# Optimization experiments

Measured on AMD Instinct MI355X. Metric: run time of the kernel, lower is better.

Reference implementation:

```python
import jax, jax.numpy as jnp
import numpy as np

N = 100000   # graph nodes
E = 600000   # edges
D = 128      # feature_dim
K = 3        # candidate ops per MixedOp
EPS = 1e-5   # BatchNorm eps


def _param_stack(key, n_ops):
    kW, kb = jax.random.split(key)
    W = jax.random.normal(kW, (n_ops, K, D, D), jnp.float32) * (1.0 / np.sqrt(D))
    b = jax.random.normal(kb, (n_ops, K, D), jnp.float32) * 0.01
    g = jnp.ones((n_ops, K, D), jnp.float32)
    be = jnp.zeros((n_ops, K, D), jnp.float32)
    return W, b, g, be


def setup_inputs() -> dict:
    key = jax.random.key(0)
    ks = jax.random.split(key, 16)
    inp = {
        'src_emb': jax.random.normal(ks[0], (N, D), jnp.float32),
        'hr': jax.random.normal(ks[1], (N, D), jnp.float32),
        'edge_src': jax.random.randint(ks[2], (E,), 0, N),
        'edge_dst': jax.random.randint(ks[3], (E,), 0, N),
        'weights_zero': jax.random.uniform(ks[4], (1, K), jnp.float32),
        'weights_first': jax.random.uniform(ks[5], (3, K), jnp.float32),
        'weights_middle': jax.random.uniform(ks[6], (2, K), jnp.float32),
        'weights_last': jax.random.uniform(ks[7], (2, K), jnp.float32),
    }
    for name, k, n_ops in [('zero', ks[8], 1), ('first', ks[9], 3), ('mid', ks[10], 2), ('last', ks[11], 2)]:
        W, b, g, be = _param_stack(k, n_ops)
        inp[f'W_{name}'] = W; inp[f'b_{name}'] = b
        inp[f'g_{name}'] = g; inp[f'be_{name}'] = be
    inp['W_cat'] = jax.random.normal(ks[12], (3 * D, D), jnp.float32) * (1.0 / np.sqrt(3 * D))
    inp['b_cat'] = jax.random.normal(ks[13], (D,), jnp.float32) * 0.01
    inp['g_cat'] = jnp.ones((D,), jnp.float32)
    inp['be_cat'] = jnp.zeros((D,), jnp.float32)
    return inp


def _mean_agg(h, src, dst):
    s = jax.ops.segment_sum(h[src], dst, num_segments=N)            # [N,D]
    deg = jax.ops.segment_sum(jnp.ones((src.shape[0],), h.dtype), dst, num_segments=N)
    return s / jnp.maximum(deg, 1.0)[:, None]


def _max_agg(h, src, dst):
    m = jax.ops.segment_max(h[src], dst, num_segments=N)            # -inf for empty segs
    return jnp.where(jnp.isfinite(m), m, 0.0)


def _mixed(cands, w, W, b, g, be):
    # cands: list of K [N,D]; w:[K]; W:[K,D,D]; b/g/be:[K,D]
    x = jnp.stack(cands)                                            # [K,N,D]
    y = jnp.einsum('knd,kdf->knf', x, W) + b[:, None, :]            # Linear per candidate
    mu = jnp.mean(y, axis=1, keepdims=True)                         # BatchNorm1d (batch stats)
    var = jnp.var(y, axis=1, keepdims=True)
    y = (y - mu) * jax.lax.rsqrt(var + EPS) * g[:, None, :] + be[:, None, :]
    y = jax.nn.relu(y)
    return jnp.einsum('k,knd->nd', w, y)                            # alpha-weighted sum


def _graph_cands(h, src, dst):
    return [h, _mean_agg(h, src, dst), _max_agg(h, src, dst)]


def _cell_forward(src_emb, hr, edge_src, edge_dst,
                  weights_zero, weights_first, weights_middle, weights_last,
                  W_zero, b_zero, g_zero, be_zero,
                  W_first, b_first, g_first, be_first,
                  W_mid, b_mid, g_mid, be_mid,
                  W_last, b_last, g_last, be_last,
                  W_cat, b_cat, g_cat, be_cat):
    src, dst = edge_src, edge_dst
    # Cell_Zero: relation-composition candidates on (src_emb, hr)
    pre = [src_emb, src_emb - hr, src_emb * hr]
    h_in = _mixed(pre, weights_zero[0], W_zero[0], b_zero[0], g_zero[0], be_zero[0])
    # Cell_First (nodes=2): ops layout [(i=0,j=0),(i=1,j=0),(i=1,j=1)]
    states = [h_in]
    s0 = _mixed(_graph_cands(states[0], src, dst), weights_first[0], W_first[0], b_first[0], g_first[0], be_first[0])
    states.append(s0)
    s1 = (_mixed(_graph_cands(states[0], src, dst), weights_first[1], W_first[1], b_first[1], g_first[1], be_first[1])
          + _mixed(_graph_cands(states[1], src, dst), weights_first[2], W_first[2], b_first[2], g_first[2], be_first[2]))
    states.append(s1)
    states = states[1:]                                             # drop h_in -> len 2
    # Cell_Middle (nodes=2): one MixedOp per state
    states = [_mixed(_graph_cands(states[i], src, dst), weights_middle[i], W_mid[i], b_mid[i], g_mid[i], be_mid[i])
              for i in range(2)]
    # Cell_Last (in_nodes=2, nodes=1): one new state from both inputs; returns all 3
    s_last = (_mixed(_graph_cands(states[0], src, dst), weights_last[0], W_last[0], b_last[0], g_last[0], be_last[0])
              + _mixed(_graph_cands(states[1], src, dst), weights_last[1], W_last[1], b_last[1], g_last[1], be_last[1]))
    states = states + [s_last]                                      # len 3
    # concat -> Linear -> BN -> ReLU (dropout p=0)
    h = jnp.concatenate(states, axis=1) @ W_cat + b_cat             # [N,D]
    mu = jnp.mean(h, axis=0, keepdims=True)
    var = jnp.var(h, axis=0, keepdims=True)
    h = (h - mu) * jax.lax.rsqrt(var + EPS) * g_cat + be_cat
    return jax.nn.relu(h)


def reference(src_emb, hr, edge_src, edge_dst,
              weights_zero, weights_first, weights_middle, weights_last,
              W_zero, b_zero, g_zero, be_zero,
              W_first, b_first, g_first, be_first,
              W_mid, b_mid, g_mid, be_mid,
              W_last, b_last, g_last, be_last,
              W_cat, b_cat, g_cat, be_cat):
    return _cell_forward(src_emb, hr, edge_src, edge_dst,
                         weights_zero, weights_first, weights_middle, weights_last,
                         W_zero, b_zero, g_zero, be_zero,
                         W_first, b_first, g_first, be_first,
                         W_mid, b_mid, g_mid, be_mid,
                         W_last, b_last, g_last, be_last,
                         W_cat, b_cat, g_cat, be_cat)
```

## Files before the change

### kernel.cpp

```cpp
#include <hip/hip_runtime.h>

#define N_NODES 100000
#define N_EDGES 600000
#define NPAD    100096
#define NTILES  782
#define SCAN_B  98
#define EPS_F   1e-5f
#define GRIDG   256

typedef __bf16 bf16_t;
typedef __bf16 bf16x8 __attribute__((ext_vector_type(8)));
typedef __bf16 bf16x4 __attribute__((ext_vector_type(4)));
typedef float  f32x4  __attribute__((ext_vector_type(4)));

__global__ __launch_bounds__(256)
void init_zero_kernel(int* __restrict__ deg, int* __restrict__ cnt)
{
    int i = blockIdx.x * 256 + threadIdx.x;
    if (i < N_NODES) deg[i] = 0;
    if (i < 32) cnt[i] = 0;
}

__global__ __launch_bounds__(256)
void transpose_w_kernel(const float* __restrict__ Wz, const float* __restrict__ Wf,
                        const float* __restrict__ Wm, const float* __restrict__ Wl,
                        const float* __restrict__ Wc, bf16_t* __restrict__ wt)
{
    int idx = blockIdx.x * 256 + threadIdx.x;
    int mat = idx >> 14;
    int off = idx & 16383;
    int n = off >> 7, kk = off & 127;
    const float* src;
    if      (mat < 3)  src = Wz + mat * 16384;
    else if (mat < 12) src = Wf + (mat - 3) * 16384;
    else if (mat < 18) src = Wm + (mat - 12) * 16384;
    else if (mat < 24) src = Wl + (mat - 18) * 16384;
    else               src = Wc + (mat - 24) * 16384;
    wt[idx] = (bf16_t)src[kk * 128 + n];
}

__global__ __launch_bounds__(256)
void pre_kernel(const float* __restrict__ se, const float* __restrict__ hr,
                bf16_t* __restrict__ p0, bf16_t* __restrict__ p1, bf16_t* __restrict__ p2)
{
    long i = ((long)blockIdx.x * 256 + threadIdx.x) * 8;
    float4 a0 = *(const float4*)&se[i], a1 = *(const float4*)&se[i + 4];
    float4 b0 = *(const float4*)&hr[i], b1 = *(const float4*)&hr[i + 4];
    float av[8] = {a0.x, a0.y, a0.z, a0.w, a1.x, a1.y, a1.z, a1.w};
    float bv[8] = {b0.x, b0.y, b0.z, b0.w, b1.x, b1.y, b1.z, b1.w};
    bf16x8 o0, o1, o2;
#pragma unroll
    for (int j = 0; j < 8; ++j) {
        o0[j] = (bf16_t)av[j];
        o1[j] = (bf16_t)(av[j] - bv[j]);
        o2[j] = (bf16_t)(av[j] * bv[j]);
    }
    *(bf16x8*)&p0[i] = o0;
    *(bf16x8*)&p1[i] = o1;
    *(bf16x8*)&p2[i] = o2;
}

__global__ __launch_bounds__(256)
void deg_count_kernel(const int* __restrict__ dst, int* __restrict__ deg)
{
    int i = blockIdx.x * 256 + threadIdx.x;
    if (i < N_EDGES) atomicAdd(&deg[dst[i]], 1);
}

__global__ __launch_bounds__(256)
void scan_a_kernel(const int* __restrict__ deg, int* __restrict__ partials)
{
    __shared__ int ls[256];
    int b = blockIdx.x, t = threadIdx.x;
    int s = 0;
    for (int j = 0; j < 4; ++j) {
        int i = b * 1024 + t * 4 + j;
        if (i < N_NODES) s += deg[i];
    }
    ls[t] = s; __syncthreads();
    for (int o = 128; o > 0; o >>= 1) {
        if (t < o) ls[t] += ls[t + o];
        __syncthreads();
    }
    if (t == 0) partials[b] = ls[0];
}

__global__ void scan_b_kernel(const int* __restrict__ partials, int* __restrict__ pofs)
{
    if (threadIdx.x == 0) {
        int a = 0;
        for (int i = 0; i < SCAN_B; ++i) { pofs[i] = a; a += partials[i]; }
    }
}

__global__ __launch_bounds__(256)
void scan_c_kernel(const int* __restrict__ deg, const int* __restrict__ pofs,
                   int* __restrict__ row_ptr, int* __restrict__ cursor)
{
    __shared__ int ls[256];
    int b = blockIdx.x, t = threadIdx.x;
    int v[4], s = 0;
    for (int j = 0; j < 4; ++j) {
        int i = b * 1024 + t * 4 + j;
        v[j] = (i < N_NODES) ? deg[i] : 0;
        s += v[j];
    }
    ls[t] = s; __syncthreads();
    for (int o = 1; o < 256; o <<= 1) {
        int tv = (t >= o) ? ls[t - o] : 0;
        __syncthreads();
        ls[t] += tv;
        __syncthreads();
    }
    int excl = ls[t] - s + pofs[b];
    for (int j = 0; j < 4; ++j) {
        int i = b * 1024 + t * 4 + j;
        if (i < N_NODES) { row_ptr[i] = excl; cursor[i] = excl; excl += v[j]; }
    }
    if (b == 0 && t == 0) row_ptr[N_NODES] = N_EDGES;
}

__global__ __launch_bounds__(256)
void scatter_kernel(const int* __restrict__ src, const int* __restrict__ dst,
                    int* __restrict__ cursor, int* __restrict__ csr_src)
{
    int i = blockIdx.x * 256 + threadIdx.x;
    if (i < N_EDGES) {
        int p = atomicAdd(&cursor[dst[i]], 1);
        csr_src[p] = src[i];
    }
}

__global__ __launch_bounds__(256)
void agg_kernel(const bf16_t* __restrict__ h, const int* __restrict__ row_ptr,
                const int* __restrict__ csr_src,
                bf16_t* __restrict__ mean_o, bf16_t* __restrict__ max_o)
{
    int node = blockIdx.x * 16 + (threadIdx.x >> 4);
    int dd = (threadIdx.x & 15) * 8;
    int e0 = row_ptr[node], e1 = row_ptr[node + 1];
    float s[8], mx[8];
#pragma unroll
    for (int j = 0; j < 8; ++j) { s[j] = 0.f; mx[j] = 0.f; }
    for (int e = e0; e < e1; ++e) {
        int sc = csr_src[e];
        bf16x8 v = *(const bf16x8*)&h[(long)sc * 128 + dd];
#pragma unroll
        for (int j = 0; j < 8; ++j) {
            float f = (float)v[j];
            s[j] += f;
            mx[j] = fmaxf(mx[j], f);
        }
    }
    float inv = 1.f / fmaxf((float)(e1 - e0), 1.f);
    bf16x8 om, ox;
#pragma unroll
    for (int j = 0; j < 8; ++j) { om[j] = (bf16_t)(s[j] * inv); ox[j] = (bf16_t)mx[j]; }
    *(bf16x8*)&mean_o[(long)node * 128 + dd] = om;
    *(bf16x8*)&max_o [(long)node * 128 + dd] = ox;
}

__device__ __forceinline__ void gload_lds16(const bf16_t* g, bf16_t* l)
{
    __builtin_amdgcn_global_load_lds(
        (const __attribute__((address_space(1))) void*)g,
        (__attribute__((address_space(3))) void*)l, 16, 0, 0);
}

__device__ __forceinline__ void barrier_lgkm()
{
    asm volatile("s_waitcnt lgkmcnt(0)" ::: "memory");
    __builtin_amdgcn_s_barrier();
    asm volatile("" ::: "memory");
}

__device__ __forceinline__ void grid_bar(int* c, int do_rel, int do_acq)
{
    __syncthreads();
    if (threadIdx.x == 0) {
        if (do_rel) __builtin_amdgcn_fence(__ATOMIC_RELEASE, "agent");
        __hip_atomic_fetch_add(c, 1, __ATOMIC_RELAXED, __HIP_MEMORY_SCOPE_AGENT);
        while (__hip_atomic_load(c, __ATOMIC_RELAXED, __HIP_MEMORY_SCOPE_AGENT) < GRIDG)
            __builtin_amdgcn_s_sleep(16);
        if (do_acq) __builtin_amdgcn_fence(__ATOMIC_ACQUIRE, "agent");
    }
    __syncthreads();
}

__global__ __launch_bounds__(512, 1)
void mixed_kernel(const bf16_t* __restrict__ x0, const bf16_t* __restrict__ x1,
                  const bf16_t* __restrict__ x2, const bf16_t* __restrict__ wt,
                  const float* __restrict__ bias, const float* __restrict__ gg,
                  const float* __restrict__ be, const float* __restrict__ wmix,
                  bf16_t* __restrict__ outb, float* __restrict__ outf,
                  float* __restrict__ partial, float* __restrict__ tmp,
                  int* __restrict__ cnt, int mode, int accflag)
{
    __shared__ __align__(16) bf16_t lds_x[4][16384];
    __shared__ float lsc[768];

    const int tid  = threadIdx.x;
    const int lane = tid & 63;
    const int w8   = tid >> 6;
    const int quad = lane >> 4;
    const int t16  = lane & 15;
    const int wr = w8 >> 2, wc = w8 & 3;
    const int bid = blockIdx.x;
    const float invN = 1.0f / (float)N_NODES;

    int srcoff[4], dsto[4];
#pragma unroll
    for (int i = 0; i < 4; ++i) {
        int ci = i * 512 + tid;
        int row = ci >> 4, c = ci & 15;
        srcoff[i] = row * 128 + ((c ^ (row & 15)) * 8);
        dsto[i]   = ci * 8;
    }
    auto stage = [&](const bf16_t* src, int slot) {
#pragma unroll
        for (int i = 0; i < 4; ++i)
            gload_lds16(src + srcoff[i], &lds_x[slot][dsto[i]]);
    };
    auto xp = [&](int c) { return (c == 0) ? x0 : (c == 1) ? x1 : x2; };

    bf16x8 wreg[3][2][4];
#pragma unroll
    for (int c = 0; c < 3; ++c)
#pragma unroll
        for (int ns = 0; ns < 2; ++ns)
#pragma unroll
            for (int ks = 0; ks < 4; ++ks)
                wreg[c][ns][ks] = *(const bf16x8*)
                    &wt[(long)c * 16384 + (wc * 32 + ns * 16 + t16) * 128
                        + ks * 32 + quad * 8];

    const int ts = (int)(((long)bid * NTILES) / GRIDG);
    const int te = (int)(((long)(bid + 1) * NTILES) / GRIDG);
    const int nk = (mode == 0) ? 3 : 1;

    f32x4 acc[2][4];
    float ssA[3][8], sqA[3][8];
#pragma unroll
    for (int k = 0; k < 3; ++k)
#pragma unroll
        for (int i = 0; i < 8; ++i) { ssA[k][i] = 0.f; sqA[k][i] = 0.f; }

#define ZACC() do { \
    _Pragma("unroll") for (int a_ = 0; a_ < 2; ++a_) \
    _Pragma("unroll") for (int b_ = 0; b_ < 4; ++b_) \
        acc[a_][b_] = (f32x4){0.f, 0.f, 0.f, 0.f}; } while (0)

#define MMAC(C) do { \
    _Pragma("unroll") for (int ks = 0; ks < 4; ++ks) { \
        bf16x8 xf[4]; \
        _Pragma("unroll") for (int ms = 0; ms < 4; ++ms) { \
            int row_ = wr * 64 + ms * 16 + t16; \
            int sw_ = (ks * 4 + quad) ^ t16; \
            xf[ms] = *(const bf16x8*)&lds_x[slot][row_ * 128 + sw_ * 8]; \
        } \
        _Pragma("unroll") for (int ns = 0; ns < 2; ++ns) \
        _Pragma("unroll") for (int ms = 0; ms < 4; ++ms) \
            acc[ns][ms] = __builtin_amdgcn_mfma_f32_16x16x32_bf16( \
                wreg[C][ns][ks], xf[ms], acc[ns][ms], 0, 0, 0); \
    } } while (0)

#define ACCST(K) do { \
    _Pragma("unroll") for (int ms = 0; ms < 4; ++ms) { \
        long m_ = (long)tile * 128 + wr * 64 + ms * 16 + t16; \
        if (m_ < N_NODES) { \
            _Pragma("unroll") for (int ns = 0; ns < 2; ++ns) \
            _Pragma("unroll") for (int j_ = 0; j_ < 4; ++j_) { \
                float v_ = acc[ns][ms][j_]; \
                ssA[K][ns * 4 + j_] += v_; \
                sqA[K][ns * 4 + j_] += v_ * v_; \
            } \
        } \
    } } while (0)

#define RINGWAIT(w_, e_) do { \
    int ah_ = (e_) - 1 - (w_); \
    if (ah_ >= 2)      asm volatile("s_waitcnt vmcnt(8)" ::: "memory"); \
    else if (ah_ == 1) asm volatile("s_waitcnt vmcnt(4)" ::: "memory"); \
    else               asm volatile("s_waitcnt vmcnt(0)" ::: "memory"); \
    __builtin_amdgcn_sched_barrier(0); \
    __builtin_amdgcn_s_barrier(); \
    __builtin_amdgcn_sched_barrier(0); } while (0)

    {
        int sA, eA;
        if (mode == 0) {
            sA = (int)(((long)bid * (NTILES * 3)) / GRIDG);
            eA = (int)(((long)(bid + 1) * (NTILES * 3)) / GRIDG);
        } else {
            sA = ts * 3; eA = te * 3;
        }
#pragma unroll 1
        for (int i = 0; i < 3; ++i)
            if (sA + i < eA) stage(xp((sA + i) % 3) + (long)((sA + i) / 3) * 16384,
                                   (sA + i) & 3);
#pragma unroll 1
        for (int w = sA; w < eA; ++w) {
            const int c = w % 3, tile = w / 3, slot = w & 3;
            RINGWAIT(w, eA);
            if (w + 3 < eA)
                stage(xp((w + 3) % 3) + (long)((w + 3) / 3) * 16384, (w + 3) & 3);
            if (mode == 0 || c == 0) ZACC();
            if (c == 0) MMAC(0); else if (c == 1) MMAC(1); else MMAC(2);
            if (mode == 0) {
                if (c == 0) ACCST(0); else if (c == 1) ACCST(1); else ACCST(2);
            } else if (c == 2) ACCST(0);
        }
    }

#pragma unroll
    for (int o = 1; o < 16; o <<= 1)
#pragma unroll
        for (int k = 0; k < 3; ++k)
#pragma unroll
            for (int i = 0; i < 8; ++i) {
                ssA[k][i] += __shfl_xor(ssA[k][i], o);
                sqA[k][i] += __shfl_xor(sqA[k][i], o);
            }
#pragma unroll 1
    for (int k = 0; k < nk; ++k) {
        barrier_lgkm();
        if (t16 == 0) {
#pragma unroll
            for (int ns = 0; ns < 2; ++ns)
#pragma unroll
                for (int i = 0; i < 4; ++i) {
                    float s_, q_;
                    if (k == 0)      { s_ = ssA[0][ns*4+i]; q_ = sqA[0][ns*4+i]; }
                    else if (k == 1) { s_ = ssA[1][ns*4+i]; q_ = sqA[1][ns*4+i]; }
                    else             { s_ = ssA[2][ns*4+i]; q_ = sqA[2][ns*4+i]; }
                    lsc[w8 * 64 +      ns * 16 + quad * 4 + i] = s_;
                    lsc[w8 * 64 + 32 + ns * 16 + quad * 4 + i] = q_;
                }
        }
        barrier_lgkm();
        if (tid < 256) {
            int selo = (tid >> 7) * 32;
            int d = tid & 127;
            int wcq = d >> 5, f = d & 31;
            float v = lsc[wcq * 64 + selo + f] + lsc[(wcq + 4) * 64 + selo + f];
            partial[((long)k * GRIDG + bid) * 256 + tid] = v;
        }
    }

    const int foldblk = (bid < nk * 16);
    grid_bar(cnt + 0, 1, foldblk);
    if (foldblk && tid < 256) {
        int k = bid >> 4, j = bid & 15;
        float s = 0.f;
        const float* pp = partial + ((long)k * GRIDG + j * 16) * 256 + tid;
#pragma unroll
        for (int b = 0; b < 16; ++b) s += pp[(long)b * 256];
        tmp[(k * 16 + j) * 256 + tid] = s;
    }
    grid_bar(cnt + 1, foldblk, 1);
    if (tid < 128) {
        for (int k = 0; k < nk; ++k) {
            float S = 0.f, Q = 0.f;
#pragma unroll
            for (int j = 0; j < 16; ++j) {
                S += tmp[(k * 16 + j) * 256 + tid];
                Q += tmp[(k * 16 + j) * 256 + 128 + tid];
            }
            float sa  = S * invN;
            float var = Q * invN - sa * sa;
            float rs  = rsqrtf(var + EPS_F);
            float gk = gg[k * 128 + tid], bek = be[k * 128 + tid];
            float wk = (mode == 0) ? wmix[k] : 1.f;
            lsc[k * 256 + tid]       = wk * rs * gk;
            lsc[k * 256 + 128 + tid] = wk * (-sa * rs * gk + bek);
        }
    }
    __syncthreads();

    {
        const int w0 = ts * 3, w1 = te * 3;
        f32x4 res[2][4];
#pragma unroll 1
        for (int i = 0; i < 3; ++i)
            if (w0 + i < w1) stage(xp((w0 + i) % 3) + (long)((w0 + i) / 3) * 16384,
                                   (w0 + i) & 3);
#pragma unroll 1
        for (int w = w0; w < w1; ++w) {
            const int c = w % 3, tile = w / 3, slot = w & 3;
            RINGWAIT(w, w1);
            if (w + 3 < w1)
                stage(xp((w + 3) % 3) + (long)((w + 3) / 3) * 16384, (w + 3) & 3);
            if (mode == 0 || c == 0) ZACC();
            if (mode == 0 && c == 0) {
                if (accflag) {
#pragma unroll
                    for (int ns = 0; ns < 2; ++ns)
#pragma unroll
                        for (int ms = 0; ms < 4; ++ms) {
                            long m = (long)tile * 128 + wr * 64 + ms * 16 + t16;
                            int n0 = wc * 32 + ns * 16 + quad * 4;
                            bf16x4 pv = *(const bf16x4*)&outb[m * 128 + n0];
                            res[ns][ms] = (f32x4){(float)pv[0], (float)pv[1],
                                                  (float)pv[2], (float)pv[3]};
                        }
                } else {
#pragma unroll
                    for (int a = 0; a < 2; ++a)
#pragma unroll
                        for (int b = 0; b < 4; ++b) res[a][b] = (f32x4){0.f, 0.f, 0.f, 0.f};
                }
            }
            if (c == 0) MMAC(0); else if (c == 1) MMAC(1); else MMAC(2);

            if (mode == 0) {
#pragma unroll
                for (int ns = 0; ns < 2; ++ns) {
                    int n0 = wc * 32 + ns * 16 + quad * 4;
                    float4 A4 = *(const float4*)&lsc[c * 256 + n0];
                    float4 B4 = *(const float4*)&lsc[c * 256 + 128 + n0];
#pragma unroll
                    for (int ms = 0; ms < 4; ++ms) {
                        res[ns][ms][0] += fmaxf(acc[ns][ms][0] * A4.x + B4.x, 0.f);
                        res[ns][ms][1] += fmaxf(acc[ns][ms][1] * A4.y + B4.y, 0.f);
                        res[ns][ms][2] += fmaxf(acc[ns][ms][2] * A4.z + B4.z, 0.f);
                        res[ns][ms][3] += fmaxf(acc[ns][ms][3] * A4.w + B4.w, 0.f);
                    }
                }
                if (c == 2) {
#pragma unroll
                    for (int ms = 0; ms < 4; ++ms) {
                        long m = (long)tile * 128 + wr * 64 + ms * 16 + t16;
                        if (m < N_NODES) {
#pragma unroll
                            for (int ns = 0; ns < 2; ++ns) {
                                int n0 = wc * 32 + ns * 16 + quad * 4;
                                bf16x4 ov;
                                ov[0] = (bf16_t)res[ns][ms][0];
                                ov[1] = (bf16_t)res[ns][ms][1];
                                ov[2] = (bf16_t)res[ns][ms][2];
                                ov[3] = (bf16_t)res[ns][ms][3];
                                *(bf16x4*)&outb[m * 128 + n0] = ov;
                            }
                        }
                    }
                }
            } else if (c == 2) {
#pragma unroll
                for (int ms = 0; ms < 4; ++ms) {
                    long m = (long)tile * 128 + wr * 64 + ms * 16 + t16;
                    if (m < N_NODES) {
#pragma unroll
                        for (int ns = 0; ns < 2; ++ns) {
                            int n0 = wc * 32 + ns * 16 + quad * 4;
                            float4 A4 = *(const float4*)&lsc[n0];
                            float4 B4 = *(const float4*)&lsc[128 + n0];
                            float4 o;
                            o.x = fmaxf(acc[ns][ms][0] * A4.x + B4.x, 0.f);
                            o.y = fmaxf(acc[ns][ms][1] * A4.y + B4.y, 0.f);
                            o.z = fmaxf(acc[ns][ms][2] * A4.z + B4.z, 0.f);
                            o.w = fmaxf(acc[ns][ms][3] * A4.w + B4.w, 0.f);
                            *(float4*)&outf[m * 128 + n0] = o;
                        }
                    }
                }
            }
        }
    }
#undef ZACC
#undef MMAC
#undef ACCST
#undef RINGWAIT
}

extern "C" void kernel_launch(void* const* d_in, const int* in_sizes, int n_in,
                              void* d_out, int out_size, void* d_ws, size_t ws_size,
                              hipStream_t stream)
{
    const float* src_emb = (const float*)d_in[0];
    const float* hr      = (const float*)d_in[1];
    const int*   e_src   = (const int*)d_in[2];
    const int*   e_dst   = (const int*)d_in[3];
    const float* w_zero  = (const float*)d_in[4];
    const float* w_first = (const float*)d_in[5];
    const float* w_mid   = (const float*)d_in[6];
    const float* w_last  = (const float*)d_in[7];
    const float* W_zero  = (const float*)d_in[8];
    const float* b_zero  = (const float*)d_in[9];
    const float* g_zero  = (const float*)d_in[10];
    const float* be_zero = (const float*)d_in[11];
    const float* W_first = (const float*)d_in[12];
    const float* b_first = (const float*)d_in[13];
    const float* g_first = (const float*)d_in[14];
    const float* be_first= (const float*)d_in[15];
    const float* W_mid   = (const float*)d_in[16];
    const float* b_mid   = (const float*)d_in[17];
    const float* g_mid   = (const float*)d_in[18];
    const float* be_mid  = (const float*)d_in[19];
    const float* W_last  = (const float*)d_in[20];
    const float* b_last  = (const float*)d_in[21];
    const float* g_last  = (const float*)d_in[22];
    const float* be_last = (const float*)d_in[23];
    const float* W_cat   = (const float*)d_in[24];
    const float* b_cat   = (const float*)d_in[25];
    const float* g_cat   = (const float*)d_in[26];
    const float* be_cat  = (const float*)d_in[27];
    float* out = (float*)d_out;

    char* ws = (char*)d_ws;
    size_t off = 0;
    auto carve = [&](size_t bytes) -> char* {
        off = (off + 255) & ~(size_t)255;
        char* p = ws + off;
        off += bytes;
        return p;
    };

    const size_t SB = (size_t)NPAD * 128 * sizeof(bf16_t);
    bf16_t* B[8];
    for (int i = 0; i < 8; ++i) B[i] = (bf16_t*)carve(SB);
    bf16_t* wt    = (bf16_t*)carve((size_t)27 * 16384 * 2);
    float*  partial = (float*)carve((size_t)3 * GRIDG * 256 * sizeof(float));
    float*  tmp   = (float*)carve((size_t)48 * 256 * sizeof(float));
    int* cnts   = (int*)carve(32 * 4);
    int* deg    = (int*)carve((size_t)N_NODES * 4);
    int* rowp   = (int*)carve((size_t)(N_NODES + 1) * 4);
    int* cursor = (int*)carve((size_t)N_NODES * 4);
    int* csr    = (int*)carve((size_t)N_EDGES * 4);
    int* parts  = (int*)carve(SCAN_B * 4);
    int* pofs   = (int*)carve(SCAN_B * 4);

    bf16_t* wtZ  = wt;
    bf16_t* wtF0 = wt + (size_t)3  * 16384;
    bf16_t* wtF1 = wt + (size_t)6  * 16384;
    bf16_t* wtF2 = wt + (size_t)9  * 16384;
    bf16_t* wtM0 = wt + (size_t)12 * 16384;
    bf16_t* wtM1 = wt + (size_t)15 * 16384;
    bf16_t* wtL0 = wt + (size_t)18 * 16384;
    bf16_t* wtL1 = wt + (size_t)21 * 16384;
    bf16_t* wtC  = wt + (size_t)24 * 16384;

    const int GEL8 = (N_NODES * 128) / 2048;

    init_zero_kernel<<<dim3((N_NODES + 255) / 256), dim3(256), 0, stream>>>(deg, cnts);
    transpose_w_kernel<<<dim3(1728), dim3(256), 0, stream>>>(W_zero, W_first, W_mid, W_last, W_cat, wt);
    deg_count_kernel<<<dim3((N_EDGES + 255) / 256), dim3(256), 0, stream>>>(e_dst, deg);
    scan_a_kernel<<<dim3(SCAN_B), dim3(256), 0, stream>>>(deg, parts);
    scan_b_kernel<<<dim3(1), dim3(64), 0, stream>>>(parts, pofs);
    scan_c_kernel<<<dim3(SCAN_B), dim3(256), 0, stream>>>(deg, pofs, rowp, cursor);
    scatter_kernel<<<dim3((N_EDGES + 255) / 256), dim3(256), 0, stream>>>(e_src, e_dst, cursor, csr);

    auto M = [&](const bf16_t* x0_, const bf16_t* x1_, const bf16_t* x2_,
                 const bf16_t* w_, const float* b_, const float* g_, const float* be_,
                 const float* wm_, bf16_t* ob_, float* of_, int acc_, int mode_, int id) {
        mixed_kernel<<<dim3(GRIDG), dim3(512), 0, stream>>>(
            x0_, x1_, x2_, w_, b_, g_, be_, wm_, ob_, of_,
            partial, tmp, cnts + id * 2, mode_, acc_);
    };
    auto A = [&](const bf16_t* h_, bf16_t* me_, bf16_t* mx_) {
        agg_kernel<<<dim3(N_NODES / 16), dim3(256), 0, stream>>>(h_, rowp, csr, me_, mx_);
    };

    pre_kernel<<<dim3(GEL8), dim3(256), 0, stream>>>(src_emb, hr, B[3], B[4], B[5]);
    M(B[3], B[4], B[5], wtZ, b_zero, g_zero, be_zero, w_zero, B[6], nullptr, 0, 0, 0);

    A(B[6], B[3], B[4]);

    M(B[6], B[3], B[4], wtF0, b_first + 0, g_first + 0, be_first + 0,
      w_first + 0, B[5], nullptr, 0, 0, 1);
    M(B[6], B[3], B[4], wtF1, b_first + 384, g_first + 384, be_first + 384,
      w_first + 3, B[7], nullptr, 0, 0, 2);

    A(B[5], B[3], B[4]);

    M(B[5], B[3], B[4], wtF2, b_first + 768, g_first + 768, be_first + 768,
      w_first + 6, B[7], nullptr, 1, 0, 3);
    M(B[5], B[3], B[4], wtM0, b_mid + 0, g_mid + 0, be_mid + 0,
      w_mid + 0, B[6], nullptr, 0, 0, 4);

    A(B[7], B[3], B[4]);

    M(B[7], B[3], B[4], wtM1, b_mid + 384, g_mid + 384, be_mid + 384,
      w_mid + 3, B[5], nullptr, 0, 0, 5);

    A(B[6], B[3], B[4]);
    M(B[6], B[3], B[4], wtL0, b_last + 0, g_last + 0, be_last + 0,
      w_last + 0, B[7], nullptr, 0, 0, 6);
    A(B[5], B[3], B[4]);
    M(B[5], B[3], B[4], wtL1, b_last + 384, g_last + 384, be_last + 384,
      w_last + 3, B[7], nullptr, 1, 0, 7);

    M(B[6], B[5], B[7], wtC, b_cat, g_cat, be_cat, nullptr,
      nullptr, out, 0, 1, 8);
}
```

Baseline: 1.163 ms.

## Restructure mixed kernel to 256-thread blocks, two per CU, with LDS-staged weights

The mixed GEMM kernel now launches 512 blocks of 256 threads, two per CU, instead of 256 blocks of 512 threads. Weights are staged through LDS for every tile rather than held in registers, so each wave computes a 64x64 output block. Per-tile BatchNorm statistics are written to a partial buffer indexed by tile, and the fold step sums over tile ranges. The four-slot asynchronous staging ring is replaced by synchronous load-then-compute with __syncthreads, so global-load latency is no longer overlapped within a block. The design relies on the second resident block per CU to hide that latency.

After: 1.465 ms. 1.26x slower.

```diff
diff --git a/kernel.cpp b/kernel.cpp
--- a/kernel.cpp
+++ b/kernel.cpp
@@ -6,7 +6,7 @@
 #define NTILES  782
 #define SCAN_B  98
 #define EPS_F   1e-5f
-#define GRIDG   256
+#define GRIDG   512
 
 typedef __bf16 bf16_t;
 typedef __bf16 bf16x8 __attribute__((ext_vector_type(8)));
@@ -187,7 +187,7 @@
     __syncthreads();
 }
 
-__global__ __launch_bounds__(512, 1)
+__global__ __launch_bounds__(256, 2)
 void mixed_kernel(const bf16_t* __restrict__ x0, const bf16_t* __restrict__ x1,
                   const bf16_t* __restrict__ x2, const bf16_t* __restrict__ wt,
                   const float* __restrict__ bias, const float* __restrict__ gg,
@@ -196,95 +196,100 @@
                   float* __restrict__ partial, float* __restrict__ tmp,
                   int* __restrict__ cnt, int mode, int accflag)
 {
-    __shared__ __align__(16) bf16_t lds_x[4][16384];
+    __shared__ __align__(16) bf16_t lds_w[16384];
+    __shared__ __align__(16) bf16_t lds_x[16384];
     __shared__ float lsc[768];
 
     const int tid  = threadIdx.x;
     const int lane = tid & 63;
-    const int w8   = tid >> 6;
+    const int wave = tid >> 6;
     const int quad = lane >> 4;
     const int t16  = lane & 15;
-    const int wr = w8 >> 2, wc = w8 & 3;
+    const int wr = wave >> 1, wc = wave & 1;
     const int bid = blockIdx.x;
     const float invN = 1.0f / (float)N_NODES;
 
-    int srcoff[4], dsto[4];
-#pragma unroll
-    for (int i = 0; i < 4; ++i) {
-        int ci = i * 512 + tid;
+    int srcoff[8], dsto[8];
+#pragma unroll
+    for (int i = 0; i < 8; ++i) {
+        int ci = i * 256 + tid;
         int row = ci >> 4, c = ci & 15;
         srcoff[i] = row * 128 + ((c ^ (row & 15)) * 8);
         dsto[i]   = ci * 8;
     }
-    auto stage = [&](const bf16_t* src, int slot) {
-#pragma unroll
-        for (int i = 0; i < 4; ++i)
-            gload_lds16(src + srcoff[i], &lds_x[slot][dsto[i]]);
+    auto stage2 = [&](const bf16_t* wsrc, const bf16_t* xsrc) {
+#pragma unroll
+        for (int i = 0; i < 8; ++i) {
+            gload_lds16(wsrc + srcoff[i], &lds_w[dsto[i]]);
+            gload_lds16(xsrc + srcoff[i], &lds_x[dsto[i]]);
+        }
     };
     auto xp = [&](int c) { return (c == 0) ? x0 : (c == 1) ? x1 : x2; };
-
-    bf16x8 wreg[3][2][4];
-#pragma unroll
-    for (int c = 0; c < 3; ++c)
-#pragma unroll
-        for (int ns = 0; ns < 2; ++ns)
-#pragma unroll
-            for (int ks = 0; ks < 4; ++ks)
-                wreg[c][ns][ks] = *(const bf16x8*)
-                    &wt[(long)c * 16384 + (wc * 32 + ns * 16 + t16) * 128
-                        + ks * 32 + quad * 8];
 
     const int ts = (int)(((long)bid * NTILES) / GRIDG);
     const int te = (int)(((long)(bid + 1) * NTILES) / GRIDG);
     const int nk = (mode == 0) ? 3 : 1;
 
-    f32x4 acc[2][4];
-    float ssA[3][8], sqA[3][8];
-#pragma unroll
-    for (int k = 0; k < 3; ++k)
-#pragma unroll
-        for (int i = 0; i < 8; ++i) { ssA[k][i] = 0.f; sqA[k][i] = 0.f; }
+    f32x4 acc[4][4];
 
 #define ZACC() do { \
-    _Pragma("unroll") for (int a_ = 0; a_ < 2; ++a_) \
+    _Pragma("unroll") for (int a_ = 0; a_ < 4; ++a_) \
     _Pragma("unroll") for (int b_ = 0; b_ < 4; ++b_) \
         acc[a_][b_] = (f32x4){0.f, 0.f, 0.f, 0.f}; } while (0)
 
-#define MMAC(C) do { \
+#define MMAC() do { \
     _Pragma("unroll") for (int ks = 0; ks < 4; ++ks) { \
-        bf16x8 xf[4]; \
+        bf16x8 xf[4], wf[4]; \
         _Pragma("unroll") for (int ms = 0; ms < 4; ++ms) { \
             int row_ = wr * 64 + ms * 16 + t16; \
             int sw_ = (ks * 4 + quad) ^ t16; \
-            xf[ms] = *(const bf16x8*)&lds_x[slot][row_ * 128 + sw_ * 8]; \
+            xf[ms] = *(const bf16x8*)&lds_x[row_ * 128 + sw_ * 8]; \
         } \
-        _Pragma("unroll") for (int ns = 0; ns < 2; ++ns) \
+        _Pragma("unroll") for (int ns = 0; ns < 4; ++ns) { \
+            int row_ = wc * 64 + ns * 16 + t16; \
+            int sw_ = (ks * 4 + quad) ^ t16; \
+            wf[ns] = *(const bf16x8*)&lds_w[row_ * 128 + sw_ * 8]; \
+        } \
+        _Pragma("unroll") for (int ns = 0; ns < 4; ++ns) \
         _Pragma("unroll") for (int ms = 0; ms < 4; ++ms) \
             acc[ns][ms] = __builtin_amdgcn_mfma_f32_16x16x32_bf16( \
-                wreg[C][ns][ks], xf[ms], acc[ns][ms], 0, 0, 0); \
+                wf[ns], xf[ms], acc[ns][ms], 0, 0, 0); \
     } } while (0)
 
-#define ACCST(K) do { \
+#define STATS(PK, TILE) do { \
+    float ss[16], sq[16]; \
+    _Pragma("unroll") for (int i = 0; i < 16; ++i) { ss[i] = 0.f; sq[i] = 0.f; } \
     _Pragma("unroll") for (int ms = 0; ms < 4; ++ms) { \
-        long m_ = (long)tile * 128 + wr * 64 + ms * 16 + t16; \
+        long m_ = (long)(TILE) * 128 + wr * 64 + ms * 16 + t16; \
         if (m_ < N_NODES) { \
-            _Pragma("unroll") for (int ns = 0; ns < 2; ++ns) \
+            _Pragma("unroll") for (int ns = 0; ns < 4; ++ns) \
             _Pragma("unroll") for (int j_ = 0; j_ < 4; ++j_) { \
                 float v_ = acc[ns][ms][j_]; \
-                ssA[K][ns * 4 + j_] += v_; \
-                sqA[K][ns * 4 + j_] += v_ * v_; \
+                ss[ns * 4 + j_] += v_; sq[ns * 4 + j_] += v_ * v_; \
             } \
         } \
+    } \
+    _Pragma("unroll") for (int o = 1; o < 16; o <<= 1) \
+    _Pragma("unroll") for (int i = 0; i < 16; ++i) { \
+        ss[i] += __shfl_xor(ss[i], o); sq[i] += __shfl_xor(sq[i], o); \
+    } \
+    if (t16 == 0) { \
+        _Pragma("unroll") for (int i = 0; i < 16; ++i) { \
+            lsc[wave * 128 + quad * 32 + i]      = ss[i]; \
+            lsc[wave * 128 + quad * 32 + 16 + i] = sq[i]; \
+        } \
+    } \
+    barrier_lgkm(); \
+    { \
+        int d   = tid & 127; \
+        int sel = (tid >> 7) * 16; \
+        int dwc = d >> 6; \
+        int q   = (d >> 2) & 3; \
+        int i   = ((d >> 4) & 3) * 4 + (d & 3); \
+        float v = lsc[(0 * 2 + dwc) * 128 + q * 32 + sel + i] \
+                + lsc[(1 * 2 + dwc) * 128 + q * 32 + sel + i]; \
+        partial[((long)(PK) * NTILES + (TILE)) * 256 + tid] = v; \
     } } while (0)
-
-#define RINGWAIT(w_, e_) do { \
-    int ah_ = (e_) - 1 - (w_); \
-    if (ah_ >= 2)      asm volatile("s_waitcnt vmcnt(8)" ::: "memory"); \
-    else if (ah_ == 1) asm volatile("s_waitcnt vmcnt(4)" ::: "memory"); \
-    else               asm volatile("s_waitcnt vmcnt(0)" ::: "memory"); \
-    __builtin_amdgcn_sched_barrier(0); \
-    __builtin_amdgcn_s_barrier(); \
-    __builtin_amdgcn_sched_barrier(0); } while (0)
 
     {
         int sA, eA;
@@ -295,66 +300,26 @@
             sA = ts * 3; eA = te * 3;
         }
 #pragma unroll 1
-        for (int i = 0; i < 3; ++i)
-            if (sA + i < eA) stage(xp((sA + i) % 3) + (long)((sA + i) / 3) * 16384,
-                                   (sA + i) & 3);
-#pragma unroll 1
         for (int w = sA; w < eA; ++w) {
-            const int c = w % 3, tile = w / 3, slot = w & 3;
-            RINGWAIT(w, eA);
-            if (w + 3 < eA)
-                stage(xp((w + 3) % 3) + (long)((w + 3) / 3) * 16384, (w + 3) & 3);
+            const int c = w % 3, tile = w / 3;
+            __syncthreads();
+            stage2(wt + (long)c * 16384, xp(c) + (long)tile * 16384);
+            __syncthreads();
             if (mode == 0 || c == 0) ZACC();
-            if (c == 0) MMAC(0); else if (c == 1) MMAC(1); else MMAC(2);
-            if (mode == 0) {
-                if (c == 0) ACCST(0); else if (c == 1) ACCST(1); else ACCST(2);
-            } else if (c == 2) ACCST(0);
-        }
-    }
-
-#pragma unroll
-    for (int o = 1; o < 16; o <<= 1)
-#pragma unroll
-        for (int k = 0; k < 3; ++k)
-#pragma unroll
-            for (int i = 0; i < 8; ++i) {
-                ssA[k][i] += __shfl_xor(ssA[k][i], o);
-                sqA[k][i] += __shfl_xor(sqA[k][i], o);
-            }
-#pragma unroll 1
-    for (int k = 0; k < nk; ++k) {
-        barrier_lgkm();
-        if (t16 == 0) {
-#pragma unroll
-            for (int ns = 0; ns < 2; ++ns)
-#pragma unroll
-                for (int i = 0; i < 4; ++i) {
-                    float s_, q_;
-                    if (k == 0)      { s_ = ssA[0][ns*4+i]; q_ = sqA[0][ns*4+i]; }
-                    else if (k == 1) { s_ = ssA[1][ns*4+i]; q_ = sqA[1][ns*4+i]; }
-                    else             { s_ = ssA[2][ns*4+i]; q_ = sqA[2][ns*4+i]; }
-                    lsc[w8 * 64 +      ns * 16 + quad * 4 + i] = s_;
-                    lsc[w8 * 64 + 32 + ns * 16 + quad * 4 + i] = q_;
-                }
-        }
-        barrier_lgkm();
-        if (tid < 256) {
-            int selo = (tid >> 7) * 32;
-            int d = tid & 127;
-            int wcq = d >> 5, f = d & 31;
-            float v = lsc[wcq * 64 + selo + f] + lsc[(wcq + 4) * 64 + selo + f];
-            partial[((long)k * GRIDG + bid) * 256 + tid] = v;
+            MMAC();
+            if (mode == 0) STATS(c, tile);
+            else if (c == 2) STATS(0, tile);
         }
     }
 
     const int foldblk = (bid < nk * 16);
     grid_bar(cnt + 0, 1, foldblk);
-    if (foldblk && tid < 256) {
+    if (foldblk) {
         int k = bid >> 4, j = bid & 15;
+        int b0 = j * 49, b1 = (b0 + 49 < NTILES) ? b0 + 49 : NTILES;
         float s = 0.f;
-        const float* pp = partial + ((long)k * GRIDG + j * 16) * 256 + tid;
-#pragma unroll
-        for (int b = 0; b < 16; ++b) s += pp[(long)b * 256];
+        const float* pp = partial + (long)k * NTILES * 256 + tid;
+        for (int b = b0; b < b1; ++b) s += pp[(long)b * 256];
         tmp[(k * 16 + j) * 256 + tid] = s;
     }
     grid_bar(cnt + 1, foldblk, 1);
@@ -378,44 +343,39 @@
     __syncthreads();
 
     {
-        const int w0 = ts * 3, w1 = te * 3;
-        f32x4 res[2][4];
+        f32x4 res[4][4];
 #pragma unroll 1
-        for (int i = 0; i < 3; ++i)
-            if (w0 + i < w1) stage(xp((w0 + i) % 3) + (long)((w0 + i) / 3) * 16384,
-                                   (w0 + i) & 3);
-#pragma unroll 1
-        for (int w = w0; w < w1; ++w) {
-            const int c = w % 3, tile = w / 3, slot = w & 3;
-            RINGWAIT(w, w1);
-            if (w + 3 < w1)
-                stage(xp((w + 3) % 3) + (long)((w + 3) / 3) * 16384, (w + 3) & 3);
-            if (mode == 0 || c == 0) ZACC();
+        for (int w = ts * 3; w < te * 3; ++w) {
+            const int c = w % 3, tile = w / 3;
+            __syncthreads();
+            stage2(wt + (long)c * 16384, xp(c) + (long)tile * 16384);
             if (mode == 0 && c == 0) {
                 if (accflag) {
 #pragma unroll
-                    for (int ns = 0; ns < 2; ++ns)
+                    for (int ns = 0; ns < 4; ++ns)
 #pragma unroll
                         for (int ms = 0; ms < 4; ++ms) {
                             long m = (long)tile * 128 + wr * 64 + ms * 16 + t16;
-                            int n0 = wc * 32 + ns * 16 + quad * 4;
+                            int n0 = wc * 64 + ns * 16 + quad * 4;
                             bf16x4 pv = *(const bf16x4*)&outb[m * 128 + n0];
                             res[ns][ms] = (f32x4){(float)pv[0], (float)pv[1],
                                                   (float)pv[2], (float)pv[3]};
                         }
                 } else {
 #pragma unroll
-                    for (int a = 0; a < 2; ++a)
+                    for (int a = 0; a < 4; ++a)
 #pragma unroll
                         for (int b = 0; b < 4; ++b) res[a][b] = (f32x4){0.f, 0.f, 0.f, 0.f};
                 }
             }
-            if (c == 0) MMAC(0); else if (c == 1) MMAC(1); else MMAC(2);
+            __syncthreads();
+            if (mode == 0 || c == 0) ZACC();
+            MMAC();
 
             if (mode == 0) {
 #pragma unroll
-                for (int ns = 0; ns < 2; ++ns) {
-                    int n0 = wc * 32 + ns * 16 + quad * 4;
+                for (int ns = 0; ns < 4; ++ns) {
+                    int n0 = wc * 64 + ns * 16 + quad * 4;
                     float4 A4 = *(const float4*)&lsc[c * 256 + n0];
                     float4 B4 = *(const float4*)&lsc[c * 256 + 128 + n0];
 #pragma unroll
@@ -432,8 +392,8 @@
                         long m = (long)tile * 128 + wr * 64 + ms * 16 + t16;
                         if (m < N_NODES) {
 #pragma unroll
-                            for (int ns = 0; ns < 2; ++ns) {
-                                int n0 = wc * 32 + ns * 16 + quad * 4;
+                            for (int ns = 0; ns < 4; ++ns) {
+                                int n0 = wc * 64 + ns * 16 + quad * 4;
                                 bf16x4 ov;
                                 ov[0] = (bf16_t)res[ns][ms][0];
                                 ov[1] = (bf16_t)res[ns][ms][1];
@@ -450,8 +410,8 @@
                     long m = (long)tile * 128 + wr * 64 + ms * 16 + t16;
                     if (m < N_NODES) {
 #pragma unroll
-                        for (int ns = 0; ns < 2; ++ns) {
-                            int n0 = wc * 32 + ns * 16 + quad * 4;
+                        for (int ns = 0; ns < 4; ++ns) {
+                            int n0 = wc * 64 + ns * 16 + quad * 4;
                             float4 A4 = *(const float4*)&lsc[n0];
                             float4 B4 = *(const float4*)&lsc[128 + n0];
                             float4 o;
@@ -468,8 +428,7 @@
     }
 #undef ZACC
 #undef MMAC
-#undef ACCST
-#undef RINGWAIT
+#undef STATS
 }
 
 extern "C" void kernel_launch(void* const* d_in, const int* in_sizes, int n_in,
@@ -519,7 +478,7 @@
     bf16_t* B[8];
     for (int i = 0; i < 8; ++i) B[i] = (bf16_t*)carve(SB);
     bf16_t* wt    = (bf16_t*)carve((size_t)27 * 16384 * 2);
-    float*  partial = (float*)carve((size_t)3 * GRIDG * 256 * sizeof(float));
+    float*  partial = (float*)carve((size_t)3 * NTILES * 256 * sizeof(float));
     float*  tmp   = (float*)carve((size_t)48 * 256 * sizeof(float));
     int* cnts   = (int*)carve(32 * 4);
     int* deg    = (int*)carve((size_t)N_NODES * 4);
@@ -552,7 +511,7 @@
     auto M = [&](const bf16_t* x0_, const bf16_t* x1_, const bf16_t* x2_,
                  const bf16_t* w_, const float* b_, const float* g_, const float* be_,
                  const float* wm_, bf16_t* ob_, float* of_, int acc_, int mode_, int id) {
-        mixed_kernel<<<dim3(GRIDG), dim3(512), 0, stream>>>(
+        mixed_kernel<<<dim3(GRIDG), dim3(256), 0, stream>>>(
             x0_, x1_, x2_, w_, b_, g_, be_, wm_, ob_, of_,
             partial, tmp, cnts + id * 2, mode_, acc_);
     };
```
